# Kernel tuning notes

Measured on AMD Instinct MI355X. Metric: run time of the kernel, lower is better.

## Reference

```python
import jax, jax.numpy as jnp
import numpy as np
import math

PS = 16            # patch size for SigmaPredictor
HID = 8            # hidden_dim
SCALE = HID ** -0.5
SIGMA_CAP = 6.0    # BoundedSoftplus threshold
EPS_S = 1e-6       # BoundedSoftplus eps


def setup_inputs() -> dict:
    key = jax.random.key(0)
    ks = jax.random.split(key, 10)
    B, C, H, W = 2, 1, 384, 384
    d_in = C * PS * PS  # 256
    r = lambda k_, sh: jax.random.normal(k_, sh, dtype=jnp.float32) * 0.1
    z = lambda sh: jnp.zeros(sh, dtype=jnp.float32)
    return {
        "x": jax.random.uniform(ks[0], (B, C, H, W), dtype=jnp.float32),
        "Wq": r(ks[1], (d_in, HID)), "bq": z((HID,)),
        "Wk": r(ks[2], (d_in, HID)), "bk": z((HID,)),
        "Wv": r(ks[3], (d_in, HID)), "bv": z((HID,)),
        "Wsq": r(ks[4], (HID, HID)), "bsq": z((HID,)),
        "Wsk": r(ks[5], (HID, HID)), "bsk": z((HID,)),
        "Wsv": r(ks[6], (HID, HID)), "bsv": z((HID,)),
        "ln_g": jnp.ones((HID,), jnp.float32), "ln_b": z((HID,)),
        "Wp": r(ks[7], (HID, 3)),
        # bias ~4 -> sigmas ~4 -> kernel size k=13 (production-scale support)
        "bp": jnp.full((3,), 4.0, dtype=jnp.float32),
    }


def _attn(q, k, v):
    a = jax.nn.softmax(jnp.einsum('bnd,bmd->bnm', q, k) * SCALE, axis=-1)
    return jnp.einsum('bnm,bmd->bnd', a, v)


def _predict_sigmas(x, Wq, bq, Wk, bk, Wv, bv, Wsq, bsq, Wsk, bsk, Wsv, bsv, ln_g, ln_b, Wp, bp):
    b, c, h, w = x.shape
    Hp, Wn = h // PS, w // PS
    # unfold into non-overlapping patches: [B, Hp*Wn, C*PS*PS]
    pat = x.reshape(b, c, Hp, PS, Wn, PS).transpose(0, 2, 4, 1, 3, 5).reshape(b, Hp * Wn, c * PS * PS)
    feats = _attn(pat @ Wq + bq, pat @ Wk + bk, pat @ Wv + bv)
    o = _attn(feats @ Wsq + bsq, feats @ Wsk + bsk, feats @ Wsv + bsv)
    mu = o.mean(-1, keepdims=True)
    var = ((o - mu) ** 2).mean(-1, keepdims=True)
    o = (o - mu) / jnp.sqrt(var + 1e-5) * ln_g + ln_b
    s = jnp.minimum(jax.nn.softplus(o @ Wp + bp), SIGMA_CAP) + EPS_S  # BoundedSoftplus
    s = s.reshape(b, Hp, Wn, 3)
    # nearest-neighbor upsample to full resolution: [B, H, W, 3]
    return jnp.repeat(jnp.repeat(s, PS, axis=1), PS, axis=2)


def _bilateral(x, s, k):
    b, c, h, w = x.shape
    sx, sy, sr = s[..., 0], s[..., 1], s[..., 2]
    half = k // 2
    xp = jnp.pad(x, ((0, 0), (0, 0), (half, half), (half, half)))
    # [B, C, H, W, k*k], dy-major to match torch unfold/meshgrid ordering
    patches = jnp.stack([xp[:, :, dy:dy + h, dx:dx + w]
                         for dy in range(k) for dx in range(k)], axis=-1)
    coords = jnp.arange(-half, half + 1, dtype=jnp.float32)
    yy, xx = jnp.meshgrid(coords, coords, indexing='ij')
    xx2 = (xx ** 2).reshape(-1)
    yy2 = (yy ** 2).reshape(-1)
    # spatial kernel [B, H, W, k*k]
    sp = jnp.exp(-xx2 / (2 * sx[..., None] ** 2) - yy2 / (2 * sy[..., None] ** 2))
    # range kernel (C == 1 branch) [B, C, H, W, k*k]
    rg = jnp.exp(-(x[..., None] - patches) ** 2 / (2 * sr[:, None, :, :, None] ** 2))
    comb = sp[:, None] * rg
    norm = comb / (comb.sum(-1, keepdims=True) + 1e-8)
    return (patches * norm).sum(-1)


def reference(x, Wq, bq, Wk, bk, Wv, bv, Wsq, bsq, Wsk, bsk, Wsv, bsv, ln_g, ln_b, Wp, bp):
    s = _predict_sigmas(x, Wq, bq, Wk, bk, Wv, bv, Wsq, bsq, Wsk, bsk, Wsv, bsv, ln_g, ln_b, Wp, bp)
    # data-dependent kernel size, computed eagerly (matches torch .item())
    m = float(jnp.maximum(s[..., 0].max(), s[..., 1].max()))
    k = int(2 * math.ceil(m + 1))
    if k % 2 == 0:
        k += 1
    return _bilateral(x, s, k)
```

## Files before the change

### kernel.cpp

```cpp
#include <hip/hip_runtime.h>

#define N_TOK 576
#define HP    24
#define PS    16
#define IMG   384
#define ATTN_SCALE 0.35355339059327373f

__global__ __launch_bounds__(256) void k_qkv1(
    const float* __restrict__ x,
    const float* __restrict__ Wq, const float* __restrict__ bq,
    const float* __restrict__ Wk, const float* __restrict__ bk,
    const float* __restrict__ Wv, const float* __restrict__ bv,
    float* __restrict__ q1, float* __restrict__ k1, float* __restrict__ v1)
{
    const int blk = blockIdx.x;
    const int b  = blk / N_TOK;
    const int n  = blk % N_TOK;
    const int py = n / HP, px = n % HP;
    const int t  = threadIdx.x;
    const int iy = t >> 4, ix = t & 15;

    const float pv = x[b*IMG*IMG + (py*PS + iy)*IMG + (px*PS + ix)];

    float acc[24];
#pragma unroll
    for (int h = 0; h < 8; ++h) {
        acc[h]      = pv * Wq[t*8 + h];
        acc[8 + h]  = pv * Wk[t*8 + h];
        acc[16 + h] = pv * Wv[t*8 + h];
    }
#pragma unroll
    for (int off = 32; off > 0; off >>= 1) {
#pragma unroll
        for (int j = 0; j < 24; ++j)
            acc[j] += __shfl_down(acc[j], off);
    }
    __shared__ float red[4][24];
    const int lane = t & 63, w = t >> 6;
    if (lane == 0) {
#pragma unroll
        for (int j = 0; j < 24; ++j) red[w][j] = acc[j];
    }
    __syncthreads();
    if (t < 24) {
        float s = red[0][t] + red[1][t] + red[2][t] + red[3][t];
        const int h = t & 7, mat = t >> 3;
        const float* bias = (mat == 0) ? bq : (mat == 1) ? bk : bv;
        float* dst = (mat == 0) ? q1 : (mat == 1) ? k1 : v1;
        dst[(b*N_TOK + n)*8 + h] = s + bias[h];
    }
}

__global__ __launch_bounds__(256) void k_attn1(
    const float* __restrict__ q1, const float* __restrict__ k1, const float* __restrict__ v1,
    const float* __restrict__ Wsq, const float* __restrict__ bsq,
    const float* __restrict__ Wsk, const float* __restrict__ bsk,
    const float* __restrict__ Wsv, const float* __restrict__ bsv,
    float* __restrict__ q2, float* __restrict__ k2, float* __restrict__ v2)
{
    const int lane = threadIdx.x & 63;
    const int wv   = threadIdx.x >> 6;
    const int tok  = blockIdx.x*4 + wv;
    const int b    = tok / N_TOK;

    float qv[8];
#pragma unroll
    for (int h = 0; h < 8; ++h) qv[h] = q1[tok*8 + h];

    const float* kb = k1 + b*N_TOK*8;
    const float* vb = v1 + b*N_TOK*8;

    float sc[9], mx = -1e30f;
#pragma unroll
    for (int ch = 0; ch < 9; ++ch) {
        const float* kp = kb + (ch*64 + lane)*8;
        float d = 0.f;
#pragma unroll
        for (int h = 0; h < 8; ++h) d += qv[h]*kp[h];
        d *= ATTN_SCALE;
        sc[ch] = d;
        mx = fmaxf(mx, d);
    }
#pragma unroll
    for (int off = 32; off > 0; off >>= 1) mx = fmaxf(mx, __shfl_xor(mx, off));

    float ssum = 0.f, o[8];
#pragma unroll
    for (int h = 0; h < 8; ++h) o[h] = 0.f;
#pragma unroll
    for (int ch = 0; ch < 9; ++ch) {
        const float p = __expf(sc[ch] - mx);
        ssum += p;
        const float* vp = vb + (ch*64 + lane)*8;
#pragma unroll
        for (int h = 0; h < 8; ++h) o[h] += p*vp[h];
    }
#pragma unroll
    for (int off = 32; off > 0; off >>= 1) {
        ssum += __shfl_xor(ssum, off);
#pragma unroll
        for (int h = 0; h < 8; ++h) o[h] += __shfl_xor(o[h], off);
    }
    const float inv = 1.f/ssum;
    float f[8];
#pragma unroll
    for (int h = 0; h < 8; ++h) f[h] = o[h]*inv;

    if (lane < 24) {
        const int mat = lane >> 3, h = lane & 7;
        const float* Wm = (mat==0)?Wsq:(mat==1)?Wsk:Wsv;
        const float* bm = (mat==0)?bsq:(mat==1)?bsk:bsv;
        float s = bm[h];
#pragma unroll
        for (int j = 0; j < 8; ++j) s += f[j]*Wm[j*8 + h];
        float* dst = (mat==0)?q2:(mat==1)?k2:v2;
        dst[tok*8 + h] = s;
    }
}

__global__ __launch_bounds__(256) void k_attn2(
    const float* __restrict__ q2, const float* __restrict__ k2, const float* __restrict__ v2,
    const float* __restrict__ ln_g, const float* __restrict__ ln_b,
    const float* __restrict__ Wp,   const float* __restrict__ bp,
    float* __restrict__ sig, int* __restrict__ smax)
{
    const int lane = threadIdx.x & 63;
    const int wv   = threadIdx.x >> 6;
    const int tok  = blockIdx.x*4 + wv;
    const int b    = tok / N_TOK;

    float qv[8];
#pragma unroll
    for (int h = 0; h < 8; ++h) qv[h] = q2[tok*8 + h];

    const float* kb = k2 + b*N_TOK*8;
    const float* vb = v2 + b*N_TOK*8;

    float sc[9], mx = -1e30f;
#pragma unroll
    for (int ch = 0; ch < 9; ++ch) {
        const float* kp = kb + (ch*64 + lane)*8;
        float d = 0.f;
#pragma unroll
        for (int h = 0; h < 8; ++h) d += qv[h]*kp[h];
        d *= ATTN_SCALE;
        sc[ch] = d;
        mx = fmaxf(mx, d);
    }
#pragma unroll
    for (int off = 32; off > 0; off >>= 1) mx = fmaxf(mx, __shfl_xor(mx, off));

    float ssum = 0.f, o[8];
#pragma unroll
    for (int h = 0; h < 8; ++h) o[h] = 0.f;
#pragma unroll
    for (int ch = 0; ch < 9; ++ch) {
        const float p = __expf(sc[ch] - mx);
        ssum += p;
        const float* vp = vb + (ch*64 + lane)*8;
#pragma unroll
        for (int h = 0; h < 8; ++h) o[h] += p*vp[h];
    }
#pragma unroll
    for (int off = 32; off > 0; off >>= 1) {
        ssum += __shfl_xor(ssum, off);
#pragma unroll
        for (int h = 0; h < 8; ++h) o[h] += __shfl_xor(o[h], off);
    }

    if (lane == 0) {
        const float inv = 1.f/ssum;
        float f[8];
        float mu = 0.f;
#pragma unroll
        for (int h = 0; h < 8; ++h) { f[h] = o[h]*inv; mu += f[h]; }
        mu *= 0.125f;
        float var = 0.f;
#pragma unroll
        for (int h = 0; h < 8; ++h) { const float d = f[h]-mu; var += d*d; }
        var *= 0.125f;
        const float rinv = rsqrtf(var + 1e-5f);
        float on[8];
#pragma unroll
        for (int h = 0; h < 8; ++h)
            on[h] = (f[h]-mu)*rinv*ln_g[h] + ln_b[h];
        float sv[3];
#pragma unroll
        for (int c = 0; c < 3; ++c) {
            float z = bp[c];
#pragma unroll
            for (int j = 0; j < 8; ++j) z += on[j]*Wp[j*3 + c];
            const float sp = (z > 20.f) ? z : log1pf(__expf(z));
            sv[c] = fminf(sp, 6.0f) + 1e-6f;
            sig[tok*3 + c] = sv[c];
        }
        atomicMax(smax, __float_as_int(fmaxf(sv[0], sv[1])));
    }
}

__global__ void k_half(const int* __restrict__ smaxi, int* __restrict__ halfp)
{
    const float m = __int_as_float(*smaxi);
    int h = (int)ceilf(m + 1.0f);
    if (h < 1) h = 1;
    if (h > 8) h = 8;
    halfp[0] = h;
}

__global__ __launch_bounds__(256) void k_bilat(
    const float* __restrict__ x, const float* __restrict__ sig,
    const int* __restrict__ halfp, float* __restrict__ out)
{
    __shared__ float tile[32*40];
    const int blk = blockIdx.x;
    const int b  = blk / N_TOK;
    const int n  = blk % N_TOK;
    const int py = n / HP, px = n % HP;
    const int tx = threadIdx.x & 15, ty = threadIdx.x >> 4;

    const int half = halfp[0];
    const float sx = sig[blk*3 + 0];
    const float sy = sig[blk*3 + 1];
    const float sr = sig[blk*3 + 2];

    const int tilew = PS + 2*half;
    const float* xb = x + b*IMG*IMG;
    for (int yy = ty; yy < tilew; yy += 16) {
        const int gy = py*PS + yy - half;
        for (int xx = tx; xx < tilew; xx += 16) {
            const int gx = px*PS + xx - half;
            float v = 0.f;
            if ((unsigned)gy < IMG && (unsigned)gx < IMG)
                v = xb[gy*IMG + gx];
            tile[yy*40 + xx] = v;
        }
    }
    __syncthreads();

    const float c  = tile[(ty+half)*40 + (tx+half)];
    const float ax = -0.5f/(sx*sx);
    const float ay = -0.5f/(sy*sy);
    const float ar = -0.5f/(sr*sr);

    float num = 0.f, den = 0.f;
    const int k = 2*half + 1;
    for (int dy = 0; dy < k; ++dy) {
        const float fy = (float)(dy - half);
        const float ey = ay*fy*fy;
        const float* row = &tile[(ty+dy)*40 + tx];
        for (int dx = 0; dx < k; ++dx) {
            const float fx = (float)(dx - half);
            const float p  = row[dx];
            const float d  = c - p;
            const float w  = __expf(ey + ax*fx*fx + ar*d*d);
            den += w;
            num += w*p;
        }
    }
    out[b*IMG*IMG + (py*PS + ty)*IMG + (px*PS + tx)] = num/(den + 1e-8f);
}

extern "C" void kernel_launch(void* const* d_in, const int* in_sizes, int n_in,
                              void* d_out, int out_size, void* d_ws, size_t ws_size,
                              hipStream_t stream)
{
    const float* x    = (const float*)d_in[0];
    const float* Wq   = (const float*)d_in[1];
    const float* bq   = (const float*)d_in[2];
    const float* Wk   = (const float*)d_in[3];
    const float* bk   = (const float*)d_in[4];
    const float* Wv   = (const float*)d_in[5];
    const float* bv   = (const float*)d_in[6];
    const float* Wsq  = (const float*)d_in[7];
    const float* bsq  = (const float*)d_in[8];
    const float* Wsk  = (const float*)d_in[9];
    const float* bsk  = (const float*)d_in[10];
    const float* Wsv  = (const float*)d_in[11];
    const float* bsv  = (const float*)d_in[12];
    const float* ln_g = (const float*)d_in[13];
    const float* ln_b = (const float*)d_in[14];
    const float* Wp   = (const float*)d_in[15];
    const float* bp   = (const float*)d_in[16];

    float* W  = (float*)d_ws;
    float* q1 = W;
    float* k1 = W +  9216;
    float* v1 = W + 18432;
    float* q2 = W + 27648;
    float* k2 = W + 36864;
    float* v2 = W + 46080;
    float* sg = W + 55296;
    int* smax = (int*)(W + 58752);
    int* halfp = smax + 1;

    hipMemsetAsync(smax, 0, 2*sizeof(int), stream);

    k_qkv1<<<2*N_TOK, 256, 0, stream>>>(x, Wq, bq, Wk, bk, Wv, bv, q1, k1, v1);
    k_attn1<<<2*N_TOK/4, 256, 0, stream>>>(q1, k1, v1, Wsq, bsq, Wsk, bsk, Wsv, bsv,
                                           q2, k2, v2);
    k_attn2<<<2*N_TOK/4, 256, 0, stream>>>(q2, k2, v2, ln_g, ln_b, Wp, bp, sg, smax);
    k_half<<<1, 1, 0, stream>>>(smax, halfp);
    k_bilat<<<2*N_TOK, 256, 0, stream>>>(x, sg, halfp, (float*)d_out);
}
```

Baseline: 142.9 us.

## Drop memset and half-size kernel, template-unroll bilateral loop, vectorize attention loads

Removes the hipMemsetAsync and the single-thread k_half launch: smax is zeroed inside k_qkv1 and the half-width is computed inside k_bilat. The bilateral inner loops are templated on the kernel half-width and dispatched through a switch, so they fully unroll with precomputed x-direction exponents. Attention loads are turned into float4 vector loads and the shared code moves into a helper. This cuts launch overhead and loop overhead, at the cost of larger code size from the eight template instances.

Result: slower. 146.7 us (+2.6%).

```diff
diff --git a/kernel.cpp b/kernel.cpp
--- a/kernel.cpp
+++ b/kernel.cpp
@@ -11,7 +11,8 @@
     const float* __restrict__ Wq, const float* __restrict__ bq,
     const float* __restrict__ Wk, const float* __restrict__ bk,
     const float* __restrict__ Wv, const float* __restrict__ bv,
-    float* __restrict__ q1, float* __restrict__ k1, float* __restrict__ v1)
+    float* __restrict__ q1, float* __restrict__ k1, float* __restrict__ v1,
+    int* __restrict__ smax)
 {
     const int blk = blockIdx.x;
     const int b  = blk / N_TOK;
@@ -19,6 +20,8 @@
     const int py = n / HP, px = n % HP;
     const int t  = threadIdx.x;
     const int iy = t >> 4, ix = t & 15;
+
+    if (blk == 0 && t == 0) smax[0] = 0;
 
     const float pv = x[b*IMG*IMG + (py*PS + iy)*IMG + (px*PS + ix)];
 
@@ -51,6 +54,54 @@
     }
 }
 
+__device__ __forceinline__ void attn_core(
+    const float* __restrict__ qp, const float* __restrict__ kb,
+    const float* __restrict__ vb, int lane, float f[8], float* ssum_out)
+{
+    const float4 qa = *(const float4*)(qp);
+    const float4 qb_ = *(const float4*)(qp + 4);
+    float qv[8] = {qa.x, qa.y, qa.z, qa.w, qb_.x, qb_.y, qb_.z, qb_.w};
+
+    float sc[9], mx = -1e30f;
+#pragma unroll
+    for (int ch = 0; ch < 9; ++ch) {
+        const float* kp = kb + (ch*64 + lane)*8;
+        const float4 ka = *(const float4*)(kp);
+        const float4 kb2 = *(const float4*)(kp + 4);
+        float d = qv[0]*ka.x + qv[1]*ka.y + qv[2]*ka.z + qv[3]*ka.w
+                + qv[4]*kb2.x + qv[5]*kb2.y + qv[6]*kb2.z + qv[7]*kb2.w;
+        d *= ATTN_SCALE;
+        sc[ch] = d;
+        mx = fmaxf(mx, d);
+    }
+#pragma unroll
+    for (int off = 32; off > 0; off >>= 1) mx = fmaxf(mx, __shfl_xor(mx, off));
+
+    float ssum = 0.f, o[8];
+#pragma unroll
+    for (int h = 0; h < 8; ++h) o[h] = 0.f;
+#pragma unroll
+    for (int ch = 0; ch < 9; ++ch) {
+        const float p = __expf(sc[ch] - mx);
+        ssum += p;
+        const float* vp = vb + (ch*64 + lane)*8;
+        const float4 va = *(const float4*)(vp);
+        const float4 vb2 = *(const float4*)(vp + 4);
+        o[0] += p*va.x;  o[1] += p*va.y;  o[2] += p*va.z;  o[3] += p*va.w;
+        o[4] += p*vb2.x; o[5] += p*vb2.y; o[6] += p*vb2.z; o[7] += p*vb2.w;
+    }
+#pragma unroll
+    for (int off = 32; off > 0; off >>= 1) {
+        ssum += __shfl_xor(ssum, off);
+#pragma unroll
+        for (int h = 0; h < 8; ++h) o[h] += __shfl_xor(o[h], off);
+    }
+    const float inv = 1.f/ssum;
+#pragma unroll
+    for (int h = 0; h < 8; ++h) f[h] = o[h]*inv;
+    *ssum_out = ssum;
+}
+
 __global__ __launch_bounds__(256) void k_attn1(
     const float* __restrict__ q1, const float* __restrict__ k1, const float* __restrict__ v1,
     const float* __restrict__ Wsq, const float* __restrict__ bsq,
@@ -63,48 +114,8 @@
     const int tok  = blockIdx.x*4 + wv;
     const int b    = tok / N_TOK;
 
-    float qv[8];
-#pragma unroll
-    for (int h = 0; h < 8; ++h) qv[h] = q1[tok*8 + h];
-
-    const float* kb = k1 + b*N_TOK*8;
-    const float* vb = v1 + b*N_TOK*8;
-
-    float sc[9], mx = -1e30f;
-#pragma unroll
-    for (int ch = 0; ch < 9; ++ch) {
-        const float* kp = kb + (ch*64 + lane)*8;
-        float d = 0.f;
-#pragma unroll
-        for (int h = 0; h < 8; ++h) d += qv[h]*kp[h];
-        d *= ATTN_SCALE;
-        sc[ch] = d;
-        mx = fmaxf(mx, d);
-    }
-#pragma unroll
-    for (int off = 32; off > 0; off >>= 1) mx = fmaxf(mx, __shfl_xor(mx, off));
-
-    float ssum = 0.f, o[8];
-#pragma unroll
-    for (int h = 0; h < 8; ++h) o[h] = 0.f;
-#pragma unroll
-    for (int ch = 0; ch < 9; ++ch) {
-        const float p = __expf(sc[ch] - mx);
-        ssum += p;
-        const float* vp = vb + (ch*64 + lane)*8;
-#pragma unroll
-        for (int h = 0; h < 8; ++h) o[h] += p*vp[h];
-    }
-#pragma unroll
-    for (int off = 32; off > 0; off >>= 1) {
-        ssum += __shfl_xor(ssum, off);
-#pragma unroll
-        for (int h = 0; h < 8; ++h) o[h] += __shfl_xor(o[h], off);
-    }
-    const float inv = 1.f/ssum;
-    float f[8];
-#pragma unroll
-    for (int h = 0; h < 8; ++h) f[h] = o[h]*inv;
+    float f[8], ssum;
+    attn_core(q1 + tok*8, k1 + b*N_TOK*8, v1 + b*N_TOK*8, lane, f, &ssum);
 
     if (lane < 24) {
         const int mat = lane >> 3, h = lane & 7;
@@ -129,51 +140,13 @@
     const int tok  = blockIdx.x*4 + wv;
     const int b    = tok / N_TOK;
 
-    float qv[8];
-#pragma unroll
-    for (int h = 0; h < 8; ++h) qv[h] = q2[tok*8 + h];
-
-    const float* kb = k2 + b*N_TOK*8;
-    const float* vb = v2 + b*N_TOK*8;
-
-    float sc[9], mx = -1e30f;
-#pragma unroll
-    for (int ch = 0; ch < 9; ++ch) {
-        const float* kp = kb + (ch*64 + lane)*8;
-        float d = 0.f;
-#pragma unroll
-        for (int h = 0; h < 8; ++h) d += qv[h]*kp[h];
-        d *= ATTN_SCALE;
-        sc[ch] = d;
-        mx = fmaxf(mx, d);
-    }
-#pragma unroll
-    for (int off = 32; off > 0; off >>= 1) mx = fmaxf(mx, __shfl_xor(mx, off));
-
-    float ssum = 0.f, o[8];
-#pragma unroll
-    for (int h = 0; h < 8; ++h) o[h] = 0.f;
-#pragma unroll
-    for (int ch = 0; ch < 9; ++ch) {
-        const float p = __expf(sc[ch] - mx);
-        ssum += p;
-        const float* vp = vb + (ch*64 + lane)*8;
-#pragma unroll
-        for (int h = 0; h < 8; ++h) o[h] += p*vp[h];
-    }
-#pragma unroll
-    for (int off = 32; off > 0; off >>= 1) {
-        ssum += __shfl_xor(ssum, off);
-#pragma unroll
-        for (int h = 0; h < 8; ++h) o[h] += __shfl_xor(o[h], off);
-    }
+    float f[8], ssum;
+    attn_core(q2 + tok*8, k2 + b*N_TOK*8, v2 + b*N_TOK*8, lane, f, &ssum);
 
     if (lane == 0) {
-        const float inv = 1.f/ssum;
-        float f[8];
         float mu = 0.f;
 #pragma unroll
-        for (int h = 0; h < 8; ++h) { f[h] = o[h]*inv; mu += f[h]; }
+        for (int h = 0; h < 8; ++h) mu += f[h];
         mu *= 0.125f;
         float var = 0.f;
 #pragma unroll
@@ -198,18 +171,42 @@
     }
 }
 
-__global__ void k_half(const int* __restrict__ smaxi, int* __restrict__ halfp)
-{
-    const float m = __int_as_float(*smaxi);
-    int h = (int)ceilf(m + 1.0f);
-    if (h < 1) h = 1;
-    if (h > 8) h = 8;
-    halfp[0] = h;
+template<int HALF>
+__device__ __forceinline__ float bilat_core(
+    const float* __restrict__ tile, int tx, int ty,
+    float ax, float ay, float ar)
+{
+    constexpr int K = 2*HALF + 1;
+    const float c = tile[(ty+HALF)*40 + (tx+HALF)];
+
+    float ex[K];
+#pragma unroll
+    for (int d = 0; d < K; ++d) {
+        const float fd = (float)(d - HALF);
+        ex[d] = ax*fd*fd;
+    }
+
+    float num = 0.f, den = 0.f;
+#pragma unroll
+    for (int dy = 0; dy < K; ++dy) {
+        const float fy = (float)(dy - HALF);
+        const float ey = ay*fy*fy;
+        const float* row = &tile[(ty+dy)*40 + tx];
+#pragma unroll
+        for (int dx = 0; dx < K; ++dx) {
+            const float p = row[dx];
+            const float d = c - p;
+            const float w = __expf(ey + ex[dx] + ar*d*d);
+            den += w;
+            num += w*p;
+        }
+    }
+    return num/(den + 1e-8f);
 }
 
 __global__ __launch_bounds__(256) void k_bilat(
     const float* __restrict__ x, const float* __restrict__ sig,
-    const int* __restrict__ halfp, float* __restrict__ out)
+    const int* __restrict__ smaxi, float* __restrict__ out)
 {
     __shared__ float tile[32*40];
     const int blk = blockIdx.x;
@@ -218,7 +215,10 @@
     const int py = n / HP, px = n % HP;
     const int tx = threadIdx.x & 15, ty = threadIdx.x >> 4;
 
-    const int half = halfp[0];
+    const float m = __int_as_float(smaxi[0]);
+    int half = (int)ceilf(m + 1.0f);
+    half = (half < 1) ? 1 : (half > 8) ? 8 : half;
+
     const float sx = sig[blk*3 + 0];
     const float sy = sig[blk*3 + 1];
     const float sr = sig[blk*3 + 2];
@@ -237,27 +237,22 @@
     }
     __syncthreads();
 
-    const float c  = tile[(ty+half)*40 + (tx+half)];
     const float ax = -0.5f/(sx*sx);
     const float ay = -0.5f/(sy*sy);
     const float ar = -0.5f/(sr*sr);
 
-    float num = 0.f, den = 0.f;
-    const int k = 2*half + 1;
-    for (int dy = 0; dy < k; ++dy) {
-        const float fy = (float)(dy - half);
-        const float ey = ay*fy*fy;
-        const float* row = &tile[(ty+dy)*40 + tx];
-        for (int dx = 0; dx < k; ++dx) {
-            const float fx = (float)(dx - half);
-            const float p  = row[dx];
-            const float d  = c - p;
-            const float w  = __expf(ey + ax*fx*fx + ar*d*d);
-            den += w;
-            num += w*p;
-        }
-    }
-    out[b*IMG*IMG + (py*PS + ty)*IMG + (px*PS + tx)] = num/(den + 1e-8f);
+    float r;
+    switch (half) {
+        case 1: r = bilat_core<1>(tile, tx, ty, ax, ay, ar); break;
+        case 2: r = bilat_core<2>(tile, tx, ty, ax, ay, ar); break;
+        case 3: r = bilat_core<3>(tile, tx, ty, ax, ay, ar); break;
+        case 4: r = bilat_core<4>(tile, tx, ty, ax, ay, ar); break;
+        case 5: r = bilat_core<5>(tile, tx, ty, ax, ay, ar); break;
+        case 6: r = bilat_core<6>(tile, tx, ty, ax, ay, ar); break;
+        case 7: r = bilat_core<7>(tile, tx, ty, ax, ay, ar); break;
+        default: r = bilat_core<8>(tile, tx, ty, ax, ay, ar); break;
+    }
+    out[b*IMG*IMG + (py*PS + ty)*IMG + (px*PS + tx)] = r;
 }
 
 extern "C" void kernel_launch(void* const* d_in, const int* in_sizes, int n_in,
@@ -291,14 +286,10 @@
     float* v2 = W + 46080;
     float* sg = W + 55296;
     int* smax = (int*)(W + 58752);
-    int* halfp = smax + 1;
-
-    hipMemsetAsync(smax, 0, 2*sizeof(int), stream);
-
-    k_qkv1<<<2*N_TOK, 256, 0, stream>>>(x, Wq, bq, Wk, bk, Wv, bv, q1, k1, v1);
+
+    k_qkv1<<<2*N_TOK, 256, 0, stream>>>(x, Wq, bq, Wk, bk, Wv, bv, q1, k1, v1, smax);
     k_attn1<<<2*N_TOK/4, 256, 0, stream>>>(q1, k1, v1, Wsq, bsq, Wsk, bsk, Wsv, bsv,
                                            q2, k2, v2);
     k_attn2<<<2*N_TOK/4, 256, 0, stream>>>(q2, k2, v2, ln_g, ln_b, Wp, bp, sg, smax);
-    k_half<<<1, 1, 0, stream>>>(smax, halfp);
-    k_bilat<<<2*N_TOK, 256, 0, stream>>>(x, sg, halfp, (float*)d_out);
-}
+    k_bilat<<<2*N_TOK, 256, 0, stream>>>(x, sg, smax, (float*)d_out);
+}
```
